# Performance work log

Measured on AMD Instinct MI355X. Metric: run time of the kernel, lower is better.

## Reference

```python
import jax, jax.numpy as jnp
import numpy as np

B, T, N_EMBD, HEAD = 8, 2048, 1024, 64


def setup_inputs() -> dict:
    key = jax.random.key(0)
    kx, kq, kk, kv = jax.random.split(key, 4)
    s = 1.0 / np.sqrt(N_EMBD)
    return {
        "x": jax.random.normal(kx, (B, T, N_EMBD), dtype=jnp.float32),
        "Wq": jax.random.normal(kq, (N_EMBD, HEAD), dtype=jnp.float32) * s,
        "Wk": jax.random.normal(kk, (N_EMBD, HEAD), dtype=jnp.float32) * s,
        "Wv": jax.random.normal(kv, (N_EMBD, HEAD), dtype=jnp.float32) * s,
    }


def reference(x, Wq, Wk, Wv):
    # x: [B, T, C] with C = n_embd
    Bs, Ts, C = x.shape
    q = jnp.einsum('btc,ch->bth', x, Wq)  # [B,T,H]
    k = jnp.einsum('btc,ch->bth', x, Wk)
    v = jnp.einsum('btc,ch->bth', x, Wv)
    # NOTE: original scales by C**-0.5 where C = n_embd (input dim), not head_size
    scale = jnp.asarray(C, x.dtype) ** -0.5
    wei = jnp.einsum('bth,bsh->bts', q, k) * scale  # [B,T,T]
    causal = jnp.tril(jnp.ones((Ts, Ts), dtype=bool))
    wei = jnp.where(causal, wei, jnp.asarray(-jnp.inf, wei.dtype))
    wei = jax.nn.softmax(wei, axis=-1)
    out = jnp.einsum('bts,bsh->bth', wei, v)  # [B,T,H]
    return out
```

## Files before the change

kernel.cpp:

```cpp
#include <hip/hip_runtime.h>
#include <hip/hip_bf16.h>
#include <math.h>

#define B_ 8
#define T_ 2048
#define C_ 1024
#define H_ 64

typedef __attribute__((ext_vector_type(8))) __bf16 bf16x8;
typedef __attribute__((ext_vector_type(4))) float f32x4;

static __device__ inline unsigned short f2bf_u(float f) {
    __bf16 b = (__bf16)f;
    return __builtin_bit_cast(unsigned short, b);
}
static __device__ inline unsigned int pack2(float lo, float hi) {
    return (unsigned int)f2bf_u(lo) | ((unsigned int)f2bf_u(hi) << 16);
}
static __device__ inline bf16x8 cvt8(float4 a, float4 b) {
    bf16x8 w;
    w[0] = (__bf16)a.x; w[1] = (__bf16)a.y; w[2] = (__bf16)a.z; w[3] = (__bf16)a.w;
    w[4] = (__bf16)b.x; w[5] = (__bf16)b.y; w[6] = (__bf16)b.z; w[7] = (__bf16)b.w;
    return w;
}

__global__ void prep_w_kernel(const float* __restrict__ Wq,
                              const float* __restrict__ Wk,
                              const float* __restrict__ Wv,
                              unsigned short* __restrict__ Wp) {
    int idx = blockIdx.x * 256 + threadIdx.x;
    if (idx >= C_ * 192) return;
    int k = idx / 192;
    int n = idx % 192;
    const float* W = (n < 64) ? Wq : (n < 128) ? Wk : Wv;
    float val = W[k * 64 + (n & 63)];
    Wp[((size_t)(k >> 5) * 192 + n) * 32 + (k & 31)] = f2bf_u(val);
}

#define XSTR 136
__global__ __launch_bounds__(256, 2) void proj_kernel(
        const float* __restrict__ x, const unsigned short* __restrict__ Wp,
        unsigned short* __restrict__ q, unsigned short* __restrict__ k,
        unsigned short* __restrict__ vT) {
    __shared__ unsigned short xb[2][32][XSTR];
    const int wave = threadIdx.x >> 6;
    const int lane = threadIdx.x & 63;
    const int col  = lane & 15;
    const int quad = lane >> 4;
    const int row0 = blockIdx.x * 32;
    const int n0   = wave * 48;

    const int srow = threadIdx.x >> 3;
    const int sf   = (threadIdx.x & 7) * 16;
    const float* sb = x + (size_t)(row0 + srow) * C_ + sf;

    f32x4 acc[6];
    #pragma unroll
    for (int i = 0; i < 6; i++) acc[i] = (f32x4){0.f, 0.f, 0.f, 0.f};

    {
        float4 t0 = *(const float4*)(sb + 0),  t1 = *(const float4*)(sb + 4);
        float4 t2 = *(const float4*)(sb + 8),  t3 = *(const float4*)(sb + 12);
        *(bf16x8*)&xb[0][srow][sf]     = cvt8(t0, t1);
        *(bf16x8*)&xb[0][srow][sf + 8] = cvt8(t2, t3);
    }
    float4 l0 = *(const float4*)(sb + 128), l1 = *(const float4*)(sb + 132);
    float4 l2 = *(const float4*)(sb + 136), l3 = *(const float4*)(sb + 140);

    const unsigned short* wb = Wp + (size_t)(n0 + col) * 32 + quad * 8;
    bf16x8 bcur0 = *(const bf16x8*)(wb);
    bf16x8 bcur1 = *(const bf16x8*)(wb + 16 * 32);
    bf16x8 bcur2 = *(const bf16x8*)(wb + 32 * 32);
    __syncthreads();

    for (int p = 0; p < 8; ++p) {
        float4 f0, f1, f2, f3;
        if (p + 2 < 8) {
            const float* s2 = sb + (p + 2) * 128;
            f0 = *(const float4*)(s2 + 0);  f1 = *(const float4*)(s2 + 4);
            f2 = *(const float4*)(s2 + 8);  f3 = *(const float4*)(s2 + 12);
        }
        #pragma unroll
        for (int ktl = 0; ktl < 4; ++ktl) {
            const int ktg = p * 4 + ktl;
            bf16x8 bn0, bn1, bn2;
            if (ktg + 1 < 32) {
                const unsigned short* wn = wb + (size_t)(ktg + 1) * 192 * 32;
                bn0 = *(const bf16x8*)(wn);
                bn1 = *(const bf16x8*)(wn + 16 * 32);
                bn2 = *(const bf16x8*)(wn + 32 * 32);
            }
            bf16x8 a0 = *(const bf16x8*)&xb[p & 1][col][ktl * 32 + quad * 8];
            bf16x8 a1 = *(const bf16x8*)&xb[p & 1][col + 16][ktl * 32 + quad * 8];
            acc[0] = __builtin_amdgcn_mfma_f32_16x16x32_bf16(a0, bcur0, acc[0], 0, 0, 0);
            acc[1] = __builtin_amdgcn_mfma_f32_16x16x32_bf16(a0, bcur1, acc[1], 0, 0, 0);
            acc[2] = __builtin_amdgcn_mfma_f32_16x16x32_bf16(a0, bcur2, acc[2], 0, 0, 0);
            acc[3] = __builtin_amdgcn_mfma_f32_16x16x32_bf16(a1, bcur0, acc[3], 0, 0, 0);
            acc[4] = __builtin_amdgcn_mfma_f32_16x16x32_bf16(a1, bcur1, acc[4], 0, 0, 0);
            acc[5] = __builtin_amdgcn_mfma_f32_16x16x32_bf16(a1, bcur2, acc[5], 0, 0, 0);
            bcur0 = bn0; bcur1 = bn1; bcur2 = bn2;
        }
        if (p + 1 < 8) {
            unsigned short* d = &xb[(p + 1) & 1][srow][sf];
            *(bf16x8*)(d)     = cvt8(l0, l1);
            *(bf16x8*)(d + 8) = cvt8(l2, l3);
            l0 = f0; l1 = f1; l2 = f2; l3 = f3;
        }
        __syncthreads();
    }

    #pragma unroll
    for (int mt = 0; mt < 2; mt++) {
        #pragma unroll
        for (int nt = 0; nt < 3; nt++) {
            f32x4 s = acc[mt * 3 + nt];
            int c = n0 + nt * 16;
            int g = c >> 6;
            if (g < 2) {
                unsigned short* dst = (g == 0) ? q : k;
                int cc = (c & 63) + col;
                int grow = row0 + mt * 16 + quad * 4;
                #pragma unroll
                for (int r = 0; r < 4; r++)
                    dst[(size_t)(grow + r) * 64 + cc] = f2bf_u(s[r]);
            } else {
                int hh = (c - 128) + col;
                int row = row0 + mt * 16;
                int bi = row >> 11, trow = (row & 2047) + quad * 4;
                ushort4 pk;
                pk.x = f2bf_u(s[0]); pk.y = f2bf_u(s[1]);
                pk.z = f2bf_u(s[2]); pk.w = f2bf_u(s[3]);
                *(ushort4*)(vT + ((size_t)bi * 64 + hh) * T_ + trow) = pk;
            }
        }
    }
}

__global__ __launch_bounds__(512, 2) void attn_kernel(
        const unsigned short* __restrict__ q, const unsigned short* __restrict__ k,
        const unsigned short* __restrict__ vT, float* __restrict__ out) {
    __shared__ unsigned int tbuf[8][2][16 * 20];
    __shared__ float so[8][16][68];
    __shared__ float sl[8][16];
    const int wave = threadIdx.x >> 6;
    const int lane = threadIdx.x & 63;
    const int col  = lane & 15;
    const int quad = lane >> 4;
    const int bi = blockIdx.x & 7;
    const int ti = 127 - (blockIdx.x >> 3);
    const int t0 = ti * 16;
    const unsigned short* qb = q  + (size_t)bi * T_ * 64;
    const unsigned short* kb = k  + (size_t)bi * T_ * 64;
    const unsigned short* vb = vT + (size_t)bi * 64 * T_;

    bf16x8 qf0 = *(const bf16x8*)(qb + (size_t)(t0 + col) * 64 + quad * 8);
    bf16x8 qf1 = *(const bf16x8*)(qb + (size_t)(t0 + col) * 64 + 32 + quad * 8);

    f32x4 o[4];
    #pragma unroll
    for (int i = 0; i < 4; i++) o[i] = (f32x4){0.f, 0.f, 0.f, 0.f};
    float lacc = 0.f;
    const float cs = 0.03125f * 1.44269504088896f;
    const int qrow = t0 + col;

    const int nit = (t0 + 47) >> 5;
    const int ci  = (nit + 7) >> 3;
    const int it0 = wave * ci;
    const int it1 = min(it0 + ci, nit);

    for (int it = it0; it < it1; ++it) {
        const int s0 = it * 32;
        bf16x8 kf00 = *(const bf16x8*)(kb + (size_t)(s0 + col) * 64 + quad * 8);
        bf16x8 kf01 = *(const bf16x8*)(kb + (size_t)(s0 + col) * 64 + 32 + quad * 8);
        bf16x8 kf10 = *(const bf16x8*)(kb + (size_t)(s0 + 16 + col) * 64 + quad * 8);
        bf16x8 kf11 = *(const bf16x8*)(kb + (size_t)(s0 + 16 + col) * 64 + 32 + quad * 8);
        f32x4 sa = (f32x4){0.f, 0.f, 0.f, 0.f};
        f32x4 sb2 = (f32x4){0.f, 0.f, 0.f, 0.f};
        sa  = __builtin_amdgcn_mfma_f32_16x16x32_bf16(kf00, qf0, sa, 0, 0, 0);
        sa  = __builtin_amdgcn_mfma_f32_16x16x32_bf16(kf01, qf1, sa, 0, 0, 0);
        sb2 = __builtin_amdgcn_mfma_f32_16x16x32_bf16(kf10, qf0, sb2, 0, 0, 0);
        sb2 = __builtin_amdgcn_mfma_f32_16x16x32_bf16(kf11, qf1, sb2, 0, 0, 0);

        float pa[4], pb[4];
        #pragma unroll
        for (int r = 0; r < 4; r++) {
            int ka = s0 + quad * 4 + r;
            pa[r] = (ka      <= qrow) ? exp2f(sa[r]  * cs) : 0.f;
            pb[r] = (ka + 16 <= qrow) ? exp2f(sb2[r] * cs) : 0.f;
            lacc += pa[r] + pb[r];
        }
        unsigned int* tb = &tbuf[wave][it & 1][0];
        *(uint2*)&tb[col * 20 + 2 * quad] =
            make_uint2(pack2(pa[0], pa[1]), pack2(pa[2], pa[3]));
        *(uint2*)&tb[col * 20 + 8 + 2 * quad] =
            make_uint2(pack2(pb[0], pb[1]), pack2(pb[2], pb[3]));
        bf16x8 pf = *(const bf16x8*)&tb[col * 20 + 4 * quad];
        #pragma unroll
        for (int ht = 0; ht < 4; ht++) {
            bf16x8 vf = *(const bf16x8*)(vb + (size_t)(ht * 16 + col) * T_ + s0 + quad * 8);
            o[ht] = __builtin_amdgcn_mfma_f32_16x16x32_bf16(vf, pf, o[ht], 0, 0, 0);
        }
    }

    lacc += __shfl_xor(lacc, 16);
    lacc += __shfl_xor(lacc, 32);
    if (quad == 0) sl[wave][col] = lacc;
    #pragma unroll
    for (int ht = 0; ht < 4; ht++)
        *(f32x4*)&so[wave][col][ht * 16 + quad * 4] = o[ht];
    __syncthreads();

    for (int e = threadIdx.x; e < 1024; e += 512) {
        int qq = e >> 6, h = e & 63;
        float L = 0.f, val = 0.f;
        #pragma unroll
        for (int w = 0; w < 8; w++) { L += sl[w][qq]; val += so[w][qq][h]; }
        out[((size_t)bi * T_ + t0 + qq) * 64 + h] = val / L;
    }
}

extern "C" void kernel_launch(void* const* d_in, const int* in_sizes, int n_in,
                              void* d_out, int out_size, void* d_ws, size_t ws_size,
                              hipStream_t stream) {
    const float* x  = (const float*)d_in[0];
    const float* Wq = (const float*)d_in[1];
    const float* Wk = (const float*)d_in[2];
    const float* Wv = (const float*)d_in[3];
    float* out = (float*)d_out;

    unsigned short* Wp  = (unsigned short*)d_ws;
    unsigned short* qws = (unsigned short*)((char*)d_ws + 0x60000);
    unsigned short* kws = (unsigned short*)((char*)d_ws + 0x60000 + 0x200000);
    unsigned short* vws = (unsigned short*)((char*)d_ws + 0x60000 + 0x400000);

    prep_w_kernel<<<(C_ * 192 + 255) / 256, 256, 0, stream>>>(Wq, Wk, Wv, Wp);
    proj_kernel<<<(B_ * T_) / 32, 256, 0, stream>>>(x, Wp, qws, kws, vws);
    attn_kernel<<<(B_ * T_) / 16, 512, 0, stream>>>(qws, kws, vws, out);
}
```

Baseline: 149.9 us.

## Process 32 query rows per attention block to reuse K/V loads

Each attention block now handles two 16-row query tiles, so every K and V fragment loaded from global memory feeds MFMAs for both tiles, halving K/V traffic per query row. The grid is halved, launch bounds ask for 4 blocks per SM, the P staging buffer is no longer double-buffered, and the cross-wave reduction is folded into a two-stage shared-memory accumulate. In exchange the per-wave register footprint and shared memory grow, there are fewer blocks for load balancing, and an extra barrier is added.

```diff
diff --git a/kernel.cpp b/kernel.cpp
--- a/kernel.cpp
+++ b/kernel.cpp
@@ -136,85 +136,128 @@
     }
 }
 
-__global__ __launch_bounds__(512, 2) void attn_kernel(
+__global__ __launch_bounds__(512, 4) void attn_kernel(
         const unsigned short* __restrict__ q, const unsigned short* __restrict__ k,
         const unsigned short* __restrict__ vT, float* __restrict__ out) {
-    __shared__ unsigned int tbuf[8][2][16 * 20];
-    __shared__ float so[8][16][68];
-    __shared__ float sl[8][16];
+    __shared__ unsigned int tbuf[8][640];
+    __shared__ float so[4][32][68];
+    __shared__ float sl[4][32];
     const int wave = threadIdx.x >> 6;
     const int lane = threadIdx.x & 63;
     const int col  = lane & 15;
     const int quad = lane >> 4;
     const int bi = blockIdx.x & 7;
-    const int ti = 127 - (blockIdx.x >> 3);
-    const int t0 = ti * 16;
+    const int m  = 63 - (blockIdx.x >> 3);
+    const int t0 = m * 32;
     const unsigned short* qb = q  + (size_t)bi * T_ * 64;
     const unsigned short* kb = k  + (size_t)bi * T_ * 64;
     const unsigned short* vb = vT + (size_t)bi * 64 * T_;
 
-    bf16x8 qf0 = *(const bf16x8*)(qb + (size_t)(t0 + col) * 64 + quad * 8);
-    bf16x8 qf1 = *(const bf16x8*)(qb + (size_t)(t0 + col) * 64 + 32 + quad * 8);
-
-    f32x4 o[4];
+    f32x4 o[2][4];
     #pragma unroll
-    for (int i = 0; i < 4; i++) o[i] = (f32x4){0.f, 0.f, 0.f, 0.f};
-    float lacc = 0.f;
+    for (int t = 0; t < 2; t++)
+        #pragma unroll
+        for (int i = 0; i < 4; i++) o[t][i] = (f32x4){0.f, 0.f, 0.f, 0.f};
+    float laccA = 0.f, laccB = 0.f;
     const float cs = 0.03125f * 1.44269504088896f;
-    const int qrow = t0 + col;
-
-    const int nit = (t0 + 47) >> 5;
+    const int qrowA = t0 + col;
+    const int qrowB = t0 + 16 + col;
+
+    const int nit = m + 2;
     const int ci  = (nit + 7) >> 3;
     const int it0 = wave * ci;
     const int it1 = min(it0 + ci, nit);
 
-    for (int it = it0; it < it1; ++it) {
-        const int s0 = it * 32;
-        bf16x8 kf00 = *(const bf16x8*)(kb + (size_t)(s0 + col) * 64 + quad * 8);
-        bf16x8 kf01 = *(const bf16x8*)(kb + (size_t)(s0 + col) * 64 + 32 + quad * 8);
-        bf16x8 kf10 = *(const bf16x8*)(kb + (size_t)(s0 + 16 + col) * 64 + quad * 8);
-        bf16x8 kf11 = *(const bf16x8*)(kb + (size_t)(s0 + 16 + col) * 64 + 32 + quad * 8);
-        f32x4 sa = (f32x4){0.f, 0.f, 0.f, 0.f};
-        f32x4 sb2 = (f32x4){0.f, 0.f, 0.f, 0.f};
-        sa  = __builtin_amdgcn_mfma_f32_16x16x32_bf16(kf00, qf0, sa, 0, 0, 0);
-        sa  = __builtin_amdgcn_mfma_f32_16x16x32_bf16(kf01, qf1, sa, 0, 0, 0);
-        sb2 = __builtin_amdgcn_mfma_f32_16x16x32_bf16(kf10, qf0, sb2, 0, 0, 0);
-        sb2 = __builtin_amdgcn_mfma_f32_16x16x32_bf16(kf11, qf1, sb2, 0, 0, 0);
-
-        float pa[4], pb[4];
-        #pragma unroll
-        for (int r = 0; r < 4; r++) {
-            int ka = s0 + quad * 4 + r;
-            pa[r] = (ka      <= qrow) ? exp2f(sa[r]  * cs) : 0.f;
-            pb[r] = (ka + 16 <= qrow) ? exp2f(sb2[r] * cs) : 0.f;
-            lacc += pa[r] + pb[r];
-        }
-        unsigned int* tb = &tbuf[wave][it & 1][0];
-        *(uint2*)&tb[col * 20 + 2 * quad] =
-            make_uint2(pack2(pa[0], pa[1]), pack2(pa[2], pa[3]));
-        *(uint2*)&tb[col * 20 + 8 + 2 * quad] =
-            make_uint2(pack2(pb[0], pb[1]), pack2(pb[2], pb[3]));
-        bf16x8 pf = *(const bf16x8*)&tb[col * 20 + 4 * quad];
-        #pragma unroll
-        for (int ht = 0; ht < 4; ht++) {
-            bf16x8 vf = *(const bf16x8*)(vb + (size_t)(ht * 16 + col) * T_ + s0 + quad * 8);
-            o[ht] = __builtin_amdgcn_mfma_f32_16x16x32_bf16(vf, pf, o[ht], 0, 0, 0);
-        }
-    }
-
-    lacc += __shfl_xor(lacc, 16);
-    lacc += __shfl_xor(lacc, 32);
-    if (quad == 0) sl[wave][col] = lacc;
-    #pragma unroll
-    for (int ht = 0; ht < 4; ht++)
-        *(f32x4*)&so[wave][col][ht * 16 + quad * 4] = o[ht];
+    if (it0 < it1) {
+        bf16x8 qA0 = *(const bf16x8*)(qb + (size_t)(t0 + col) * 64 + quad * 8);
+        bf16x8 qA1 = *(const bf16x8*)(qb + (size_t)(t0 + col) * 64 + 32 + quad * 8);
+        bf16x8 qB0 = *(const bf16x8*)(qb + (size_t)(t0 + 16 + col) * 64 + quad * 8);
+        bf16x8 qB1 = *(const bf16x8*)(qb + (size_t)(t0 + 16 + col) * 64 + 32 + quad * 8);
+        unsigned int* tb = &tbuf[wave][0];
+
+        for (int it = it0; it < it1; ++it) {
+            const int s0 = it * 32;
+            bf16x8 kf00 = *(const bf16x8*)(kb + (size_t)(s0 + col) * 64 + quad * 8);
+            bf16x8 kf01 = *(const bf16x8*)(kb + (size_t)(s0 + col) * 64 + 32 + quad * 8);
+            bf16x8 kf10 = *(const bf16x8*)(kb + (size_t)(s0 + 16 + col) * 64 + quad * 8);
+            bf16x8 kf11 = *(const bf16x8*)(kb + (size_t)(s0 + 16 + col) * 64 + 32 + quad * 8);
+            bf16x8 vf[4];
+            #pragma unroll
+            for (int ht = 0; ht < 4; ht++)
+                vf[ht] = *(const bf16x8*)(vb + (size_t)(ht * 16 + col) * T_ + s0 + quad * 8);
+
+            f32x4 saA = (f32x4){0.f, 0.f, 0.f, 0.f};
+            f32x4 sbA = (f32x4){0.f, 0.f, 0.f, 0.f};
+            f32x4 saB = (f32x4){0.f, 0.f, 0.f, 0.f};
+            f32x4 sbB = (f32x4){0.f, 0.f, 0.f, 0.f};
+            saA = __builtin_amdgcn_mfma_f32_16x16x32_bf16(kf00, qA0, saA, 0, 0, 0);
+            saA = __builtin_amdgcn_mfma_f32_16x16x32_bf16(kf01, qA1, saA, 0, 0, 0);
+            sbA = __builtin_amdgcn_mfma_f32_16x16x32_bf16(kf10, qA0, sbA, 0, 0, 0);
+            sbA = __builtin_amdgcn_mfma_f32_16x16x32_bf16(kf11, qA1, sbA, 0, 0, 0);
+            saB = __builtin_amdgcn_mfma_f32_16x16x32_bf16(kf00, qB0, saB, 0, 0, 0);
+            saB = __builtin_amdgcn_mfma_f32_16x16x32_bf16(kf01, qB1, saB, 0, 0, 0);
+            sbB = __builtin_amdgcn_mfma_f32_16x16x32_bf16(kf10, qB0, sbB, 0, 0, 0);
+            sbB = __builtin_amdgcn_mfma_f32_16x16x32_bf16(kf11, qB1, sbB, 0, 0, 0);
+
+            float pa[4], pb[4], pc[4], pd[4];
+            #pragma unroll
+            for (int r = 0; r < 4; r++) {
+                int ka = s0 + quad * 4 + r;
+                pa[r] = (ka      <= qrowA) ? exp2f(saA[r] * cs) : 0.f;
+                pb[r] = (ka + 16 <= qrowA) ? exp2f(sbA[r] * cs) : 0.f;
+                pc[r] = (ka      <= qrowB) ? exp2f(saB[r] * cs) : 0.f;
+                pd[r] = (ka + 16 <= qrowB) ? exp2f(sbB[r] * cs) : 0.f;
+                laccA += pa[r] + pb[r];
+                laccB += pc[r] + pd[r];
+            }
+            *(uint2*)&tb[col * 20 + 2 * quad] =
+                make_uint2(pack2(pa[0], pa[1]), pack2(pa[2], pa[3]));
+            *(uint2*)&tb[col * 20 + 8 + 2 * quad] =
+                make_uint2(pack2(pb[0], pb[1]), pack2(pb[2], pb[3]));
+            *(uint2*)&tb[320 + col * 20 + 2 * quad] =
+                make_uint2(pack2(pc[0], pc[1]), pack2(pc[2], pc[3]));
+            *(uint2*)&tb[320 + col * 20 + 8 + 2 * quad] =
+                make_uint2(pack2(pd[0], pd[1]), pack2(pd[2], pd[3]));
+            bf16x8 pfA = *(const bf16x8*)&tb[col * 20 + 4 * quad];
+            bf16x8 pfB = *(const bf16x8*)&tb[320 + col * 20 + 4 * quad];
+            #pragma unroll
+            for (int ht = 0; ht < 4; ht++) {
+                o[0][ht] = __builtin_amdgcn_mfma_f32_16x16x32_bf16(vf[ht], pfA, o[0][ht], 0, 0, 0);
+                o[1][ht] = __builtin_amdgcn_mfma_f32_16x16x32_bf16(vf[ht], pfB, o[1][ht], 0, 0, 0);
+            }
+        }
+    }
+
+    laccA += __shfl_xor(laccA, 16); laccA += __shfl_xor(laccA, 32);
+    laccB += __shfl_xor(laccB, 16); laccB += __shfl_xor(laccB, 32);
+
+    if (wave >= 4) {
+        int s = wave - 4;
+        #pragma unroll
+        for (int t = 0; t < 2; t++)
+            #pragma unroll
+            for (int ht = 0; ht < 4; ht++)
+                *(f32x4*)&so[s][t * 16 + col][ht * 16 + quad * 4] = o[t][ht];
+        if (quad == 0) { sl[s][col] = laccA; sl[s][16 + col] = laccB; }
+    }
     __syncthreads();
-
-    for (int e = threadIdx.x; e < 1024; e += 512) {
+    if (wave < 4) {
+        #pragma unroll
+        for (int t = 0; t < 2; t++)
+            #pragma unroll
+            for (int ht = 0; ht < 4; ht++) {
+                f32x4 cur = *(f32x4*)&so[wave][t * 16 + col][ht * 16 + quad * 4];
+                cur += o[t][ht];
+                *(f32x4*)&so[wave][t * 16 + col][ht * 16 + quad * 4] = cur;
+            }
+        if (quad == 0) { sl[wave][col] += laccA; sl[wave][16 + col] += laccB; }
+    }
+    __syncthreads();
+
+    for (int e = threadIdx.x; e < 2048; e += 512) {
         int qq = e >> 6, h = e & 63;
-        float L = 0.f, val = 0.f;
-        #pragma unroll
-        for (int w = 0; w < 8; w++) { L += sl[w][qq]; val += so[w][qq][h]; }
+        float L = sl[0][qq] + sl[1][qq] + sl[2][qq] + sl[3][qq];
+        float val = so[0][qq][h] + so[1][qq][h] + so[2][qq][h] + so[3][qq][h];
         out[((size_t)bi * T_ + t0 + qq) * 64 + h] = val / L;
     }
 }
@@ -235,5 +278,5 @@
 
     prep_w_kernel<<<(C_ * 192 + 255) / 256, 256, 0, stream>>>(Wq, Wk, Wv, Wp);
     proj_kernel<<<(B_ * T_) / 32, 256, 0, stream>>>(x, Wp, qws, kws, vws);
-    attn_kernel<<<(B_ * T_) / 16, 512, 0, stream>>>(qws, kws, vws, out);
-}
+    attn_kernel<<<(B_ * T_) / 32, 512, 0, stream>>>(qws, kws, vws, out);
+}
```

Measured after the change: 139.8 us. 1.07x faster.
